# Performance work log

Hardware: AMD Instinct MI355X
Metric: run time of the kernel (lower is better)

Reference implementation:

```python
import jax, jax.numpy as jnp
import numpy as np

B, S, T, H, NH, G, E, I, R, L = 256, 256, 16, 1024, 8, 3, 8, 4096, 256, 3
GTEMP, RTEMP, TOPK_G, NEG = 1.0, 1.0, 2, -1e9

_W = {
    'ts_in_w': (3*H, H), 'ts_out_w': (H, H),
    'st_in_w': (3*H, H), 'st_out_w': (H, H),
    'ca_in_w': (3*H, H), 'ca_out_w': (H, H),
    'opq_w': (H, H), 'fuse_w': (H, 3*H), 'gate_w': (H, 3*H),
    'bs_w': (R, H), 'bt_w': (R, H), 'bo_w': (H, R),
    'cond_w': (H, 2*H), 'gr_w': (G, H), 'er_w': (G, E, H),
    'e_w1': (G, E, I, H), 'e_w2': (G, E, H, I), 'cls_w': (L, H),
}
_B = {
    'ts_in_b': (3*H,), 'ts_out_b': (H,), 'st_in_b': (3*H,), 'st_out_b': (H,),
    'ca_in_b': (3*H,), 'ca_out_b': (H,), 'fuse_b': (H,), 'gate_b': (H,),
    'bs_b': (R,), 'bt_b': (R,), 'bo_b': (H,), 'cond_b': (H,),
    'gr_b': (G,), 'er_b': (G, E), 'e_b1': (G, E, I), 'e_b2': (G, E, H),
    'cls_b': (L,), 'ln_b': (3*H,),
}


def setup_inputs() -> dict:
    key = jax.random.key(0)
    out = {}
    out['h_sent'] = jax.random.normal(jax.random.fold_in(key, 1), (B, S, H), dtype=jnp.float32)
    out['h_term'] = jax.random.normal(jax.random.fold_in(key, 2), (B, T, H), dtype=jnp.float32)
    for i, (name, shp) in enumerate(_W.items()):
        out[name] = 0.02 * jax.random.normal(jax.random.fold_in(key, 100 + i), shp, dtype=jnp.float32)
    for name, shp in _B.items():
        out[name] = jnp.zeros(shp, dtype=jnp.float32)
    out['ln_g'] = jnp.ones((3*H,), dtype=jnp.float32)
    return out


def _mha(q, k, v, w_in, b_in, w_out, b_out):
    # torch nn.MultiheadAttention (batch_first, eval mode / no dropout)
    wq, wk, wv = jnp.split(w_in, 3, axis=0)
    bq, bk, bv = jnp.split(b_in, 3, axis=0)
    Q, K, V = q @ wq.T + bq, k @ wk.T + bk, v @ wv.T + bv
    b, lq, _ = Q.shape
    lk = K.shape[1]
    d = H // NH
    Q = Q.reshape(b, lq, NH, d).transpose(0, 2, 1, 3)
    K = K.reshape(b, lk, NH, d).transpose(0, 2, 1, 3)
    V = V.reshape(b, lk, NH, d).transpose(0, 2, 1, 3)
    att = jax.nn.softmax(jnp.einsum('bhqd,bhkd->bhqk', Q, K) * (1.0 / d ** 0.5), axis=-1)
    o = jnp.einsum('bhqk,bhkd->bhqd', att, V).transpose(0, 2, 1, 3).reshape(b, lq, H)
    return o @ w_out.T + b_out


def _ln(x, g, b, eps=1e-5):
    mu = x.mean(-1, keepdims=True)
    var = ((x - mu) ** 2).mean(-1, keepdims=True)
    return (x - mu) * jax.lax.rsqrt(var + eps) * g + b


def reference(h_sent, h_term, ts_in_w, ts_in_b, ts_out_w, ts_out_b,
              st_in_w, st_in_b, st_out_w, st_out_b,
              ca_in_w, ca_in_b, ca_out_w, ca_out_b,
              opq_w, ln_g, ln_b, fuse_w, fuse_b, gate_w, gate_b,
              bs_w, bs_b, bt_w, bt_b, bo_w, bo_b, cond_w, cond_b,
              gr_w, gr_b, er_w, er_b, e_w1, e_b1, e_w2, e_b2, cls_w, cls_b):
    # --- co-attention fusion ---
    t2s = _mha(h_term, h_sent, h_sent, ts_in_w, ts_in_b, ts_out_w, ts_out_b)  # [B,T,H]
    s2t = _mha(h_sent, h_term, h_term, st_in_w, st_in_b, st_out_w, st_out_b)  # [B,S,H]
    v_term = t2s.mean(axis=1)   # [B,H]
    v_sent = s2t.mean(axis=1)   # [B,H]
    oq = h_term @ opq_w.T       # opinion query projection (no bias)
    v_op = _mha(oq, h_sent, h_sent, ca_in_w, ca_in_b, ca_out_w, ca_out_b).mean(axis=1)
    cat3 = jnp.concatenate([v_sent, v_term, v_op], axis=-1)        # [B,3H]
    fused_lin = _ln(cat3, ln_g, ln_b) @ fuse_w.T + fuse_b           # [B,H]
    g = jax.nn.sigmoid(cat3 @ gate_w.T + gate_b)                    # [B,H]
    bil = ((v_sent @ bs_w.T + bs_b) * (v_term @ bt_w.T + bt_b)) @ bo_w.T + bo_b
    fused = g * fused_lin + (1.0 - g) * bil                         # [B,H]
    cond = jnp.concatenate([fused, v_term], axis=-1) @ cond_w.T + cond_b  # [B,H]
    # --- hierarchical group -> expert soft routing ---
    glog = fused @ gr_w.T + gr_b                                    # [B,G]
    thr = jax.lax.top_k(glog, TOPK_G)[0][:, -1:]
    glog = jnp.where(glog >= thr, glog, NEG)
    gp = jax.nn.softmax(glog / GTEMP, axis=-1)                      # [B,G]
    elog = jnp.einsum('bh,geh->bge', cond, er_w) + er_b             # [B,G,E]
    ep = jax.nn.softmax(elog / RTEMP, axis=-1)
    # all experts applied densely (soft routing); FFN experts: GELU MLP
    h1 = jax.nn.gelu(jnp.einsum('bh,geih->bgei', fused, e_w1) + e_b1, approximate=False)
    y = jnp.einsum('bgei,gehi->bgeh', h1, e_w2) + e_b2              # [B,G,E,H]
    moe = jnp.einsum('bge,bgeh->bh', gp[:, :, None] * ep, y)
    out = fused + moe                                               # residual merge
    return out @ cls_w.T + cls_b                                    # [B,L]
```

## Files before the change

kernel.cpp:

```cpp
#include <hip/hip_runtime.h>
#include <math.h>


#define B_    256
#define S_    256
#define T_    16
#define H_    1024
#define NH_   8
#define DH_   128
#define M128_ 128
#define G_    3
#define E_    8
#define I_    4096
#define R_    256
#define L_    3
#define GE_   24

using bf16x8 = __attribute__((ext_vector_type(8))) __bf16;
using f32x4  = __attribute__((ext_vector_type(4))) float;

__device__ inline float wave_sum(float v) {
    for (int o = 32; o > 0; o >>= 1) v += __shfl_xor(v, o);
    return v;
}
__device__ inline float wave_max(float v) {
    for (int o = 32; o > 0; o >>= 1) v = fmaxf(v, __shfl_xor(v, o));
    return v;
}

template <int ACT, int NCH>
__global__ __launch_bounds__(256) void sgemm2_k(
    const float* __restrict__ Ap, const float* __restrict__ Bp,
    const float* __restrict__ biasp, const float* __restrict__ roffp,
    float* __restrict__ Cf,
    int K, int m2shift, int zshift, int z2max,
    long sA1, long sA2, long sAz1, long sAz2,
    long ldb, long sBz1, long sBz2, long sBia1, long sBia2,
    long sC1, long sC2, long sCz1, long sCz2, long sR1, long sR2,
    float scale)
{
    const int z  = blockIdx.z;
    const int z1 = z >> zshift;
    const int z2 = z & ((1 << zshift) - 1);
    if (z2 >= z2max) return;
    const int m2mask = (1 << m2shift) - 1;
    const int row0 = blockIdx.y * 128;
    const float* Ab = Ap + (long)z1 * sAz1 + (long)z2 * sAz2;
    const float* Bb = Bp + (long)z1 * sBz1 + (long)z2 * sBz2;
    const float* biasb = biasp ? biasp + (long)z1 * sBia1 + (long)z2 * sBia2 : nullptr;
    const float* roffb = roffp ? roffp + (long)z1 * sR1 + (long)z2 * sR2 : nullptr;

    __shared__ __bf16 Ahs[128 * 40];
    __shared__ __bf16 Als[128 * 40];
    __shared__ __bf16 Bhs[128 * 40];
    __shared__ __bf16 Bls[128 * 40];

    const int tid  = threadIdx.x;
    const int lane = tid & 63;
    const int wid  = tid >> 6;
    const int wm = (wid >> 1) * 64;
    const int wn = (wid & 1) * 64;
    const int fr  = lane & 15;
    const int fkb = (lane >> 4) * 16;
    const int qrow = tid >> 2;
    const int c4   = tid & 3;

    float4 pfa[2][2], pfb[2][2];

    auto loadAB = [&](int k0, int col0) {
#pragma unroll
        for (int rep = 0; rep < 2; ++rep) {
            const int row = qrow + rep * 64;
            const int r = row0 + row;
            const int r1 = r >> m2shift, r2 = r & m2mask;
            const float* srcA = Ab + (long)r1 * sA1 + (long)r2 * sA2 + k0 + c4 * 8;
            pfa[rep][0] = *(const float4*)srcA;
            pfa[rep][1] = *(const float4*)(srcA + 4);
            const float* srcB = Bb + (long)(col0 + row) * ldb + k0 + c4 * 8;
            pfb[rep][0] = *(const float4*)srcB;
            pfb[rep][1] = *(const float4*)(srcB + 4);
        }
    };

    for (int ch = 0; ch < NCH; ++ch) {
        const int col0 = (blockIdx.x * NCH + ch) * 128;
        f32x4 acc[4][4] = {};
        loadAB(0, col0);
        for (int k0 = 0; k0 < K; k0 += 32) {
            __syncthreads();
#pragma unroll
            for (int rep = 0; rep < 2; ++rep) {
                const int row = qrow + rep * 64;
                {
                    const float fv[8] = {pfa[rep][0].x, pfa[rep][0].y, pfa[rep][0].z, pfa[rep][0].w,
                                         pfa[rep][1].x, pfa[rep][1].y, pfa[rep][1].z, pfa[rep][1].w};
                    bf16x8 hi, lo;
#pragma unroll
                    for (int j = 0; j < 8; ++j) {
                        const __bf16 h = (__bf16)fv[j];
                        hi[j] = h; lo[j] = (__bf16)(fv[j] - (float)h);
                    }
                    *(bf16x8*)&Ahs[row * 40 + c4 * 8] = hi;
                    *(bf16x8*)&Als[row * 40 + c4 * 8] = lo;
                }
                {
                    const float fv[8] = {pfb[rep][0].x, pfb[rep][0].y, pfb[rep][0].z, pfb[rep][0].w,
                                         pfb[rep][1].x, pfb[rep][1].y, pfb[rep][1].z, pfb[rep][1].w};
                    bf16x8 hi, lo;
#pragma unroll
                    for (int j = 0; j < 8; ++j) {
                        const __bf16 h = (__bf16)fv[j];
                        hi[j] = h; lo[j] = (__bf16)(fv[j] - (float)h);
                    }
                    *(bf16x8*)&Bhs[row * 40 + c4 * 8] = hi;
                    *(bf16x8*)&Bls[row * 40 + c4 * 8] = lo;
                }
            }
            __syncthreads();
            if (k0 + 32 < K) loadAB(k0 + 32, col0);

            bf16x8 bh4[4], bl4[4];
#pragma unroll
            for (int n = 0; n < 4; ++n) {
                bh4[n] = *(const bf16x8*)((const char*)&Bhs[(wn + n * 16 + fr) * 40] + fkb);
                bl4[n] = *(const bf16x8*)((const char*)&Bls[(wn + n * 16 + fr) * 40] + fkb);
            }
#pragma unroll
            for (int m = 0; m < 4; ++m) {
                const bf16x8 ah = *(const bf16x8*)((const char*)&Ahs[(wm + m * 16 + fr) * 40] + fkb);
                const bf16x8 al = *(const bf16x8*)((const char*)&Als[(wm + m * 16 + fr) * 40] + fkb);
#pragma unroll
                for (int n = 0; n < 4; ++n) {
                    acc[m][n] = __builtin_amdgcn_mfma_f32_16x16x32_bf16(ah, bh4[n], acc[m][n], 0, 0, 0);
                    acc[m][n] = __builtin_amdgcn_mfma_f32_16x16x32_bf16(ah, bl4[n], acc[m][n], 0, 0, 0);
                    acc[m][n] = __builtin_amdgcn_mfma_f32_16x16x32_bf16(al, bh4[n], acc[m][n], 0, 0, 0);
                }
            }
        }

        float* Cfb = Cf + (long)z1 * sCz1 + (long)z2 * sCz2;
        const int lr4 = (lane >> 4) * 4;
#pragma unroll
        for (int m = 0; m < 4; ++m) {
#pragma unroll
            for (int r = 0; r < 4; ++r) {
                const int rr = row0 + wm + m * 16 + lr4 + r;
                const int r1 = rr >> m2shift, r2 = rr & m2mask;
                const float ro = roffb ? roffb[rr] : 0.f;
                const long cb = (long)r1 * sC1 + (long)r2 * sC2;
#pragma unroll
                for (int n = 0; n < 4; ++n) {
                    const int cc = col0 + wn + n * 16 + fr;
                    float v = (acc[m][n][r] + ro) * scale;
                    if (biasp) v += biasb[cc];
                    if (ACT == 2) v = 1.0f / (1.0f + expf(-v));
                    Cfb[cb + cc] = v;
                }
            }
        }
    }
}

static void sg2(hipStream_t s, int act, int nch, int z2max,
                const float* A, const float* B, const float* bias, const float* roff,
                float* C, int gx, int gy, int gz,
                int K, int m2shift, int zshift,
                long sA1, long sA2, long sAz1, long sAz2,
                long ldb, long sBz1, long sBz2, long sBia1, long sBia2,
                long sC1, long sC2, long sCz1, long sCz2, long sR1, long sR2,
                float scale)
{
    dim3 g(gx, gy, gz), b(256);
#define S2ARGS A, B, bias, roff, C, K, m2shift, zshift, z2max, sA1, sA2, sAz1, sAz2, \
               ldb, sBz1, sBz2, sBia1, sBia2, sC1, sC2, sCz1, sCz2, sR1, sR2, scale
    if (nch == 2)      sgemm2_k<0, 2><<<g, b, 0, s>>>(S2ARGS);
    else if (act == 2) sgemm2_k<2, 1><<<g, b, 0, s>>>(S2ARGS);
    else               sgemm2_k<0, 1><<<g, b, 0, s>>>(S2ARGS);
#undef S2ARGS
}

template <int ABF16, int BSING, int ACT, int WMUL, int OUTH>
__global__ __launch_bounds__(512) void sgemm256_k(
    const void* __restrict__ Ap, const float* __restrict__ Bp,
    const float* __restrict__ biasp, const float* __restrict__ wmulp,
    float* __restrict__ Cf, __bf16* __restrict__ Ch,
    int K, long sA1, long sAz, long ldb, long sBz, long sBz2, int bzshift,
    long sBias, long sC1, long sCz, long sWr, float scale)
{
    const int z    = blockIdx.z;
    const int col0 = blockIdx.x * 128;
    const int z1 = z >> bzshift;
    const int z2 = z - (z1 << bzshift);
    const float* Bb = Bp + (long)z1 * sBz + (long)z2 * sBz2;
    const float* biasb = biasp ? biasp + (long)z1 * sBias : nullptr;

    __shared__ __bf16 Ah[256 * 40];
    __shared__ __bf16 Al[ABF16 ? 64 : 256 * 40];
    __shared__ __bf16 Bh[128 * 40];
    __shared__ __bf16 Bl[BSING ? 64 : 128 * 40];

    const int tid  = threadIdx.x;
    const int lane = tid & 63;
    const int wid  = tid >> 6;
    const int wm = (wid >> 1) * 64;
    const int wn = (wid & 1) * 64;
    const int fr  = lane & 15;
    const int fkb = (lane >> 4) * 16;

    f32x4 acc[4][4] = {};
    bf16x8 pfah[2];
    float4 pfaf[2][2];
    float4 pfb[2];

    auto loadAB = [&](int k0) {
#pragma unroll
        for (int rep = 0; rep < 2; ++rep) {
            const int idx = tid + rep * 512;
            const int row = idx >> 2;
            const int cc4 = idx & 3;
            if (ABF16) {
                pfah[rep] = *(const bf16x8*)((const __bf16*)Ap + (long)z * sAz +
                                             (long)row * sA1 + k0 + cc4 * 8);
            } else {
                const float* src = (const float*)Ap + (long)z * sAz +
                                   (long)row * sA1 + k0 + cc4 * 8;
                pfaf[rep][0] = *(const float4*)src;
                pfaf[rep][1] = *(const float4*)(src + 4);
            }
        }
        {
            const int row = tid >> 2;
            const int cc4 = tid & 3;
            const float* src = Bb + (long)(col0 + row) * ldb + k0 + cc4 * 8;
            pfb[0] = *(const float4*)src;
            pfb[1] = *(const float4*)(src + 4);
        }
    };

    loadAB(0);
    for (int k0 = 0; k0 < K; k0 += 32) {
        __syncthreads();
#pragma unroll
        for (int rep = 0; rep < 2; ++rep) {
            const int idx = tid + rep * 512;
            const int row = idx >> 2;
            const int cc4 = idx & 3;
            if (ABF16) {
                *(bf16x8*)&Ah[row * 40 + cc4 * 8] = pfah[rep];
            } else {
                const float fv[8] = {pfaf[rep][0].x, pfaf[rep][0].y, pfaf[rep][0].z, pfaf[rep][0].w,
                                     pfaf[rep][1].x, pfaf[rep][1].y, pfaf[rep][1].z, pfaf[rep][1].w};
                bf16x8 hi, lo;
#pragma unroll
                for (int j = 0; j < 8; ++j) {
                    const __bf16 h = (__bf16)fv[j];
                    hi[j] = h; lo[j] = (__bf16)(fv[j] - (float)h);
                }
                *(bf16x8*)&Ah[row * 40 + cc4 * 8] = hi;
                *(bf16x8*)&Al[row * 40 + cc4 * 8] = lo;
            }
        }
        {
            const int row = tid >> 2;
            const int cc4 = tid & 3;
            const float fv[8] = {pfb[0].x, pfb[0].y, pfb[0].z, pfb[0].w,
                                 pfb[1].x, pfb[1].y, pfb[1].z, pfb[1].w};
            bf16x8 hi, lo;
#pragma unroll
            for (int j = 0; j < 8; ++j) {
                const __bf16 h = (__bf16)fv[j];
                hi[j] = h;
                if (!BSING) lo[j] = (__bf16)(fv[j] - (float)h);
            }
            *(bf16x8*)&Bh[row * 40 + cc4 * 8] = hi;
            if (!BSING) *(bf16x8*)&Bl[row * 40 + cc4 * 8] = lo;
        }
        __syncthreads();
        if (k0 + 32 < K) loadAB(k0 + 32);

        bf16x8 bh4[4], bl4[4];
#pragma unroll
        for (int n = 0; n < 4; ++n) {
            bh4[n] = *(const bf16x8*)((const char*)&Bh[(wn + n * 16 + fr) * 40] + fkb);
            if (!BSING) bl4[n] = *(const bf16x8*)((const char*)&Bl[(wn + n * 16 + fr) * 40] + fkb);
        }
#pragma unroll
        for (int m = 0; m < 4; ++m) {
            const bf16x8 ah = *(const bf16x8*)((const char*)&Ah[(wm + m * 16 + fr) * 40] + fkb);
            bf16x8 al;
            if (!ABF16) al = *(const bf16x8*)((const char*)&Al[(wm + m * 16 + fr) * 40] + fkb);
#pragma unroll
            for (int n = 0; n < 4; ++n) {
                acc[m][n] = __builtin_amdgcn_mfma_f32_16x16x32_bf16(ah, bh4[n], acc[m][n], 0, 0, 0);
                if (!BSING) acc[m][n] = __builtin_amdgcn_mfma_f32_16x16x32_bf16(ah, bl4[n], acc[m][n], 0, 0, 0);
                if (!ABF16) acc[m][n] = __builtin_amdgcn_mfma_f32_16x16x32_bf16(al, bh4[n], acc[m][n], 0, 0, 0);
            }
        }
    }

    const int lr4 = (lane >> 4) * 4;
#pragma unroll
    for (int m = 0; m < 4; ++m) {
#pragma unroll
        for (int r = 0; r < 4; ++r) {
            const int rr = wm + m * 16 + lr4 + r;
#pragma unroll
            for (int n = 0; n < 4; ++n) {
                const int cc = col0 + wn + n * 16 + fr;
                float v = acc[m][n][r] * scale;
                if (biasp) v += biasb[cc];
                if (ACT == 1) v = 0.5f * v * (1.0f + erff(v * 0.70710678118654752f));
                if (WMUL) v *= wmulp[(long)rr * sWr + z];
                if (OUTH) Ch[(long)z * sCz + (long)rr * sC1 + cc] = (__bf16)v;
                else      Cf[(long)z * sCz + (long)rr * sC1 + cc] = v;
            }
        }
    }
}

#define BM 64
#define BN 64
#define BK 16
__global__ __launch_bounds__(256) void gemm_k(
    const float* __restrict__ Ap, const float* __restrict__ Bp,
    const float* __restrict__ biasp, float* __restrict__ Cp,
    int M, int N, int K, long sA1, long ldb, long sC1)
{
    const int row0 = blockIdx.y * BM;
    const int col0 = blockIdx.x * BN;
    const int tid = threadIdx.x;
    __shared__ float As[BK][BM + 4];
    __shared__ float Bs[BK][BN + 4];
    float acc[4][4] = {};
    const int tm = (tid >> 4) << 2;
    const int tn = (tid & 15) << 2;
    for (int k0 = 0; k0 < K; k0 += BK) {
        {
            const int i = tid << 2;
            const int m = i >> 4, kk = i & 15;
            const int r = row0 + m;
            float4 v = make_float4(0.f, 0.f, 0.f, 0.f);
            if (r < M) v = *(const float4*)(Ap + (long)r * sA1 + k0 + kk);
            As[kk + 0][m] = v.x; As[kk + 1][m] = v.y;
            As[kk + 2][m] = v.z; As[kk + 3][m] = v.w;
        }
        {
            const int i = tid << 2;
            const int n = i >> 4, kk = i & 15;
            const int c = col0 + n;
            float4 v = make_float4(0.f, 0.f, 0.f, 0.f);
            if (c < N) v = *(const float4*)(Bp + (long)c * ldb + k0 + kk);
            Bs[kk + 0][n] = v.x; Bs[kk + 1][n] = v.y;
            Bs[kk + 2][n] = v.z; Bs[kk + 3][n] = v.w;
        }
        __syncthreads();
#pragma unroll
        for (int kk = 0; kk < BK; ++kk) {
            const float4 av = *(const float4*)&As[kk][tm];
            const float4 bv = *(const float4*)&Bs[kk][tn];
            acc[0][0] += av.x * bv.x; acc[0][1] += av.x * bv.y;
            acc[0][2] += av.x * bv.z; acc[0][3] += av.x * bv.w;
            acc[1][0] += av.y * bv.x; acc[1][1] += av.y * bv.y;
            acc[1][2] += av.y * bv.z; acc[1][3] += av.y * bv.w;
            acc[2][0] += av.z * bv.x; acc[2][1] += av.z * bv.y;
            acc[2][2] += av.z * bv.z; acc[2][3] += av.z * bv.w;
            acc[3][0] += av.w * bv.x; acc[3][1] += av.w * bv.y;
            acc[3][2] += av.w * bv.z; acc[3][3] += av.w * bv.w;
        }
        __syncthreads();
    }
#pragma unroll
    for (int i2 = 0; i2 < 4; ++i2) {
        const int r = row0 + tm + i2;
        if (r >= M) continue;
        float* crow = Cp + (long)r * sC1;
#pragma unroll
        for (int j = 0; j < 4; ++j) {
            const int c = col0 + tn + j;
            if (c >= N) continue;
            float v = acc[i2][j];
            if (biasp) v += biasp[c];
            crow[c] = v;
        }
    }
}

static void g_launch(hipStream_t s, const float* A, const float* Bw, const float* bias,
                     float* C, int M, int N, int K, long sA1, long ldb, long sC1)
{
    dim3 grid((N + BN - 1) / BN, (M + BM - 1) / BM, 1);
    gemm_k<<<grid, dim3(256), 0, s>>>(A, Bw, bias, C, M, N, K, sA1, ldb, sC1);
}

template <int ACT>
__global__ void kred_k(const float* __restrict__ part, const float* __restrict__ bias,
                       float* __restrict__ out, int n, long stride, int nz, int biasMask)
{
    const int i = blockIdx.x * blockDim.x + threadIdx.x;
    if (i >= n) return;
    float v = 0.f;
    for (int z = 0; z < nz; ++z) v += part[(long)z * stride + i];
    if (bias) v += bias[i & biasMask];
    if (ACT == 2) v = 1.0f / (1.0f + expf(-v));
    out[i] = v;
}

__global__ void cpy8_k(const float* s0, const float* s1, const float* s2, const float* s3,
                       const float* s4, const float* s5, const float* s6, const float* s7,
                       float* d0, float* d1, float* d2, float* d3,
                       float* d4, float* d5, float* d6, float* d7)
{
    const int seg = blockIdx.x >> 10;
    const int i = ((blockIdx.x & 1023) * 256 + threadIdx.x);
    const float* srcs[8] = {s0, s1, s2, s3, s4, s5, s6, s7};
    float* dsts[8] = {d0, d1, d2, d3, d4, d5, d6, d7};
    ((float4*)dsts[seg])[i] = ((const float4*)srcs[seg])[i];
}

__global__ void tT4_k(const float* s0, const float* s1, const float* s2, const float* s3,
                      float* d0, float* d1, float* d2, float* d3)
{
    __shared__ float t[32][33];
    const int seg = blockIdx.y >> 5;
    const float* src = seg == 0 ? s0 : seg == 1 ? s1 : seg == 2 ? s2 : s3;
    float* dst = seg == 0 ? d0 : seg == 1 ? d1 : seg == 2 ? d2 : d3;
    const int c0 = blockIdx.x * 32, r0 = (blockIdx.y & 31) * 32;
    const int tx = threadIdx.x & 31, ty = threadIdx.x >> 5;
#pragma unroll
    for (int i = 0; i < 4; ++i) {
        const int r = ty + i * 8;
        t[r][tx] = src[(long)(r0 + r) * 1024 + c0 + tx];
    }
    __syncthreads();
#pragma unroll
    for (int i = 0; i < 4; ++i) {
        const int r = ty + i * 8;
        dst[(long)(c0 + r) * 1024 + r0 + tx] = t[tx][r];
    }
}

__global__ void biascat_k(const float* __restrict__ ts_b, const float* __restrict__ ca_b,
                          const float* __restrict__ st_b,
                          const float* __restrict__ ts_ob, const float* __restrict__ ca_ob,
                          const float* __restrict__ st_ob,
                          float* __restrict__ BCAT, float* __restrict__ BKCAT,
                          float* __restrict__ WVB, float* __restrict__ WOB)
{
    const int i = blockIdx.x * blockDim.x + threadIdx.x;
    if (i >= 1024) return;
    BCAT[i] = ts_b[i]; BCAT[1024 + i] = ca_b[i];
    BCAT[2048 + i] = st_b[1024 + i]; BCAT[3072 + i] = st_b[2048 + i];
    BKCAT[i] = ts_b[1024 + i]; BKCAT[1024 + i] = ca_b[1024 + i]; BKCAT[2048 + i] = st_b[i];
    WVB[i] = ts_b[2048 + i]; WVB[1024 + i] = ca_b[2048 + i];
    WOB[i] = ts_ob[i]; WOB[1024 + i] = ca_ob[i]; WOB[2048 + i] = st_ob[i];
}

__global__ void headdot3_k(const float* __restrict__ QALL, const float* __restrict__ BKCAT,
                           float* __restrict__ out)
{
    const int idx = blockIdx.x * blockDim.x + threadIdx.x;
    if (idx >= 3 * B_ * T_ * NH_) return;
    const int mod = idx >> 15;
    const int b = (idx >> 7) & 255;
    const int t = (idx >> 3) & 15;
    const int h = idx & 7;
    const float* q = QALL + (long)(b * 16 + t) * 4096 + mod * 1024 + h * 128;
    const float* bb = BKCAT + mod * 1024 + h * 128;
    float sum = 0.f;
    for (int k = 0; k < DH_; ++k) sum += q[k] * bb[k];
    out[idx] = sum;
}

__global__ __launch_bounds__(64) void softpb_k(const float* __restrict__ sc3,
                                               float* __restrict__ pbar,
// ... 203 lines not shown
    for (int e = 0; e < E_; ++e) { v[e] = expf(p[e] - m); sum += v[e]; }
    const float w = gp[idx] / sum;
#pragma unroll
    for (int e = 0; e < E_; ++e) p[e] = v[e] * w;
}

__global__ void moefinal_k(const float* __restrict__ part, const float* __restrict__ fused,
                           const float* __restrict__ wsc, const float* __restrict__ e_b2,
                           float* __restrict__ res)
{
    const int idx = blockIdx.x * blockDim.x + threadIdx.x;
    if (idx >= B_ * H_) return;
    const int b = idx >> 10;
    const int h = idx & (H_ - 1);
    float acc = fused[idx];
#pragma unroll 8
    for (int z = 0; z < 48; ++z) acc += part[(long)z * (B_ * H_) + idx];
    float ba = 0.f;
#pragma unroll
    for (int ge = 0; ge < GE_; ++ge) ba += wsc[b * GE_ + ge] * e_b2[ge * H_ + h];
    res[idx] = acc + ba;
}

extern "C" void kernel_launch(void* const* d_in, const int* in_sizes, int n_in,
                              void* d_out, int out_size, void* d_ws, size_t ws_size,
                              hipStream_t stream)
{
    const float* h_sent  = (const float*)d_in[0];
    const float* h_term  = (const float*)d_in[1];
    const float* ts_in_w = (const float*)d_in[2];
    const float* ts_out_w= (const float*)d_in[3];
    const float* st_in_w = (const float*)d_in[4];
    const float* st_out_w= (const float*)d_in[5];
    const float* ca_in_w = (const float*)d_in[6];
    const float* ca_out_w= (const float*)d_in[7];
    const float* opq_w   = (const float*)d_in[8];
    const float* fuse_w  = (const float*)d_in[9];
    const float* gate_w  = (const float*)d_in[10];
    const float* bs_w    = (const float*)d_in[11];
    const float* bt_w    = (const float*)d_in[12];
    const float* bo_w    = (const float*)d_in[13];
    const float* cond_w  = (const float*)d_in[14];
    const float* gr_w    = (const float*)d_in[15];
    const float* er_w    = (const float*)d_in[16];
    const float* e_w1    = (const float*)d_in[17];
    const float* e_w2    = (const float*)d_in[18];
    const float* cls_w   = (const float*)d_in[19];
    const float* ts_in_b = (const float*)d_in[20];
    const float* ts_out_b= (const float*)d_in[21];
    const float* st_in_b = (const float*)d_in[22];
    const float* st_out_b= (const float*)d_in[23];
    const float* ca_in_b = (const float*)d_in[24];
    const float* ca_out_b= (const float*)d_in[25];
    const float* fuse_b  = (const float*)d_in[26];
    const float* gate_b  = (const float*)d_in[27];
    const float* bs_b    = (const float*)d_in[28];
    const float* bt_b    = (const float*)d_in[29];
    const float* bo_b    = (const float*)d_in[30];
    const float* cond_b  = (const float*)d_in[31];
    const float* gr_b    = (const float*)d_in[32];
    const float* er_b    = (const float*)d_in[33];
    const float* e_b1    = (const float*)d_in[34];
    const float* e_b2    = (const float*)d_in[35];
    const float* cls_b   = (const float*)d_in[36];
    const float* ln_b    = (const float*)d_in[37];
    const float* ln_g    = (const float*)d_in[38];
    (void)in_sizes; (void)n_in; (void)out_size; (void)ws_size;

    float* ws = (float*)d_ws;
    size_t off = 0;
    auto allocF = [&](size_t n) { float* p = ws + off; off += (n + 63) & ~(size_t)63; return p; };

    float* QALL  = allocF(16777216);
    float* WCAT  = allocF(4194304);
    float* BCAT  = allocF(4096);
    float* BKCAT = allocF(3072);
    float* wT3   = allocF(3145728);
    float* opqT  = allocF(1048576);
    float* WVCAT = allocF(2097152);
    float* WVB   = allocF(2048);
    float* WOCAT = allocF(3145728);
    float* WOB   = allocF(3072);
    float* OFFS3 = allocF(98304);
    float* BIG3  = allocF(100663296);
    float* SC3   = allocF(25165824);
    float* PBAR3 = allocF(1048576);
    float* CTXB3 = allocF(4194304);
    float* PARTC = allocF(16777216);
    float* OBAR3 = allocF(786432);
    float* VOUT3 = allocF(786432);
    float* ATTM  = allocF(32768);
    float* CAT3  = allocF(786432);
    float* LNC   = allocF(786432);
    float* FLIN  = allocF(262144);
    float* GATE  = allocF(262144);
    float* BSV   = allocF(65536);
    float* BTV   = allocF(65536);
    float* PROD  = allocF(65536);
    float* BIL   = allocF(262144);
    float* FUSED = allocF(262144);
    float* FUSEDH= allocF(131072);
    float* CATFV = allocF(524288);
    float* COND  = allocF(262144);
    float* GLOG  = allocF(1024);
    float* GP    = allocF(1024);
    float* ELOG  = allocF(8192);
    float* RES   = allocF(262144);
    float* PARTF = allocF(1048576);
    float* H1Wf  = allocF(12582912);
    float* PART  = allocF(12582912);
    __bf16* FUSEDbf = (__bf16*)FUSEDH;
    __bf16* H1W     = (__bf16*)H1Wf;
    float* VTERM = VOUT3;
    float* VOP   = VOUT3 + 262144;
    float* VSENT = VOUT3 + 524288;

    hipStream_t s = stream;
    const float rscale = 0.08838834764831845f;
    const int ZBIG = 1 << 30;

    cpy8_k<<<dim3(8 * 1024), dim3(256), 0, s>>>(
        ts_in_w, st_in_w + 1048576, st_in_w + 2097152, ts_in_w + 2097152,
        ca_in_w + 2097152, ts_out_w, ca_out_w, st_out_w,
        WCAT, WCAT + 2097152, WCAT + 3145728, WVCAT,
        WVCAT + 1048576, WOCAT, WOCAT + 1048576, WOCAT + 2097152);
    biascat_k<<<dim3(4), dim3(256), 0, s>>>(ts_in_b, ca_in_b, st_in_b,
                                            ts_out_b, ca_out_b, st_out_b,
                                            BCAT, BKCAT, WVB, WOB);
    tT4_k<<<dim3(32, 128), dim3(256), 0, s>>>(
        ts_in_w + 1048576, ca_in_w + 1048576, st_in_w, opq_w,
        wT3, wT3 + 1048576, wT3 + 2097152, opqT);

    sg2(s, 0, 1, ZBIG, ca_in_w, opqT, nullptr, nullptr, WCAT + 1048576,
        8, 8, 1, 1024, 12, 0, 0, 1024, 0, 0, 1024, 0, 0, 0, 0,
        0, 1024, 0, 0, 0, 0, 1.f);

    sg2(s, 0, 1, ZBIG, h_term, WCAT, BCAT, nullptr, QALL,
        32, 32, 1, 1024, 12, 0, 0, 1024, 0, 0, 1024, 0, 0, 0, 0,
        0, 4096, 0, 0, 0, 0, 1.f);

    headdot3_k<<<dim3(384), dim3(256), 0, s>>>(QALL, BKCAT, OFFS3);

    sg2(s, 0, 1, ZBIG, QALL, wT3, nullptr, nullptr, BIG3,
        8, 32, 24, 128, 4, 3,
        65536, 4096, 1024, 128,
        1024, 1048576, 128, 0, 0,
        131072, 8192, 33554432, 1024, 0, 0, 1.f);

    sg2(s, 0, 2, 3, BIG3, h_sent, nullptr, OFFS3, SC3,
        1, 1, 1024, 1024, 12, 2,
        0, 1024, 131072, 33554432,
        1024, 262144, 0, 0, 0,
        0, 256, 32768, 8388608, 128, 32768, rscale);

    softpb_k<<<dim3(3 * B_ * NH_), dim3(64), 0, s>>>(SC3, PBAR3, ATTM);

    ctxw2_k<<<dim3(B_, 4), dim3(256), 0, s>>>(PBAR3, h_sent, PARTC);
    kred_k<0><<<dim3(4194304 / 256), dim3(256), 0, s>>>(PARTC, nullptr, CTXB3,
                                                        4194304, 4194304, 4, 0);
    sg2(s, 0, 1, ZBIG, CTXB3, WVCAT, WVB, nullptr, OBAR3,
        1, 2, 16, 1024, 12, 3,
        0, 8192, 2097152, 1024,
        1024, 1048576, 131072, 1024, 128,
        0, 1024, 262144, 128, 0, 0, 1.f);

    ohead2_k<<<dim3((B_ * H_ + 255) / 256), dim3(256), 0, s>>>(ATTM, QALL, OBAR3 + 524288);

    sg2(s, 0, 1, ZBIG, OBAR3, WOCAT, WOB, nullptr, VOUT3,
        8, 2, 3, 1024, 12, 0,
        0, 1024, 262144, 0,
        1024, 1048576, 0, 1024, 0,
        0, 1024, 262144, 0, 0, 0, 1.f);

    cat3_k<<<dim3((B_ * 3 * H_ + 255) / 256), dim3(256), 0, s>>>(VSENT, VTERM, VOP, CAT3);
    ln_k<<<dim3(B_), dim3(256), 0, s>>>(CAT3, ln_g, ln_b, LNC);
    sg2(s, 0, 1, ZBIG, LNC, fuse_w, nullptr, nullptr, PARTF,
        8, 2, 4, 768, 12, 2, 0, 3072, 0, 768, 3072, 0, 768, 0, 0,
        0, 1024, 0, 262144, 0, 0, 1.f);
    kred_k<0><<<dim3(1024), dim3(256), 0, s>>>(PARTF, fuse_b, FLIN, 262144, 262144, 4, 1023);
    sg2(s, 0, 1, ZBIG, CAT3, gate_w, nullptr, nullptr, PARTF,
        8, 2, 4, 768, 12, 2, 0, 3072, 0, 768, 3072, 0, 768, 0, 0,
        0, 1024, 0, 262144, 0, 0, 1.f);
    kred_k<2><<<dim3(1024), dim3(256), 0, s>>>(PARTF, gate_b, GATE, 262144, 262144, 4, 1023);
    sg2(s, 0, 1, ZBIG, VSENT, bs_w, nullptr, nullptr, PARTF,
        2, 2, 4, 256, 12, 2, 0, 1024, 0, 256, 1024, 0, 256, 0, 0,
        0, 256, 0, 65536, 0, 0, 1.f);
    kred_k<0><<<dim3(256), dim3(256), 0, s>>>(PARTF, bs_b, BSV, 65536, 65536, 4, 255);
    sg2(s, 0, 1, ZBIG, VTERM, bt_w, nullptr, nullptr, PARTF,
        2, 2, 4, 256, 12, 2, 0, 1024, 0, 256, 1024, 0, 256, 0, 0,
        0, 256, 0, 65536, 0, 0, 1.f);
    kred_k<0><<<dim3(256), dim3(256), 0, s>>>(PARTF, bt_b, BTV, 65536, 65536, 4, 255);
    mulf_k<<<dim3((B_ * R_ + 255) / 256), dim3(256), 0, s>>>(BSV, BTV, PROD, B_ * R_);
    sg2(s, 0, 1, ZBIG, PROD, bo_w, nullptr, nullptr, PARTF,
        8, 2, 2, 128, 12, 1, 0, 256, 0, 128, 256, 0, 128, 0, 0,
        0, 1024, 0, 262144, 0, 0, 1.f);
    kred_k<0><<<dim3(1024), dim3(256), 0, s>>>(PARTF, bo_b, BIL, 262144, 262144, 2, 1023);
    fuse_k<<<dim3((B_ * H_ + 255) / 256), dim3(256), 0, s>>>(GATE, FLIN, BIL, FUSED, FUSEDbf);
    catfv_k<<<dim3((B_ * 2 * H_ + 255) / 256), dim3(256), 0, s>>>(FUSED, VTERM, CATFV);
    sg2(s, 0, 1, ZBIG, CATFV, cond_w, nullptr, nullptr, PARTF,
        8, 2, 4, 512, 12, 2, 0, 2048, 0, 512, 2048, 0, 512, 0, 0,
        0, 1024, 0, 262144, 0, 0, 1.f);
    kred_k<0><<<dim3(1024), dim3(256), 0, s>>>(PARTF, cond_b, COND, 262144, 262144, 4, 1023);

    g_launch(s, FUSED, gr_w, gr_b, GLOG, B_, G_, H_, H_, H_, G_);
    route_k<<<dim3(1), dim3(256), 0, s>>>(GLOG, GP);
    g_launch(s, COND, er_w, er_b, ELOG, B_, GE_, H_, H_, H_, GE_);
    epsm_k<<<dim3(3), dim3(256), 0, s>>>(ELOG, GP);

    sgemm256_k<1, 1, 1, 1, 1><<<dim3(I_ / 128, 1, GE_), dim3(512), 0, s>>>(
        FUSEDbf, e_w1, e_b1, ELOG, nullptr, H1W,
        1024, H_, 0, H_, (long)I_ * H_, 0, 0, I_,
        (long)GE_ * I_, I_, GE_, 1.f);
    sgemm256_k<1, 1, 0, 0, 0><<<dim3(H_ / 128, 1, 2 * GE_), dim3(512), 0, s>>>(
        H1W, e_w2, nullptr, nullptr, PART, nullptr,
        2048, (long)GE_ * I_, 2048, I_, (long)H_ * I_, 2048, 1, 0,
        H_, (long)B_ * H_, 0, 1.f);
    moefinal_k<<<dim3(B_ * H_ / 256), dim3(256), 0, s>>>(PART, FUSED, ELOG, e_b2, RES);

    g_launch(s, RES, cls_w, cls_b, (float*)d_out, B_, L_, H_, H_, H_, L_);
}
```

Before: 1.627 ms.

## Fuse projected-query and score GEMMs into one kernel, replace tiny GEMMs with dot kernels

Merges the two-stage score computation (QALL×wT3 into a large BIG3 buffer, then BIG3×h_sent) into a single fsc_k kernel. Each block computes its 128×64 projected tile in registers and keeps it in LDS as split bf16, so the roughly 400 MB intermediate is never written to or read back from global memory. The small routing and classifier GEMMs (N=3 or 24) move from a 64×64-tiled SIMT GEMM to one-wave-per-output dot-product kernels. Side changes: the NCH/z2max paths are removed from sgemm2_k and the bf16 hi/lo split is factored into a helper. The risk is that the fused kernel redoes the projection per block, uses a 512-thread launch with large LDS, and has a quarter of its blocks exit immediately.

```diff
diff --git a/kernel.cpp b/kernel.cpp
--- a/kernel.cpp
+++ b/kernel.cpp
@@ -28,12 +28,135 @@
     return v;
 }
 
-template <int ACT, int NCH>
+__device__ inline void split8(const float4& f0, const float4& f1, bf16x8& hi, bf16x8& lo)
+{
+    const float fv[8] = {f0.x, f0.y, f0.z, f0.w, f1.x, f1.y, f1.z, f1.w};
+#pragma unroll
+    for (int j = 0; j < 8; ++j) {
+        const __bf16 h = (__bf16)fv[j];
+        hi[j] = h; lo[j] = (__bf16)(fv[j] - (float)h);
+    }
+}
+
+__global__ __launch_bounds__(512) void fsc_k(
+    const float* __restrict__ QALL, const float* __restrict__ wT3,
+    const float* __restrict__ hs, const float* __restrict__ OFFS3,
+    float* __restrict__ SC3, float rscale)
+{
+    const int zz = ((blockIdx.z & 7) << 7) | (blockIdx.z >> 3);
+    const int b = zz >> 2, mod = zz & 3;
+    if (mod == 3) return;
+
+    __shared__ __bf16 A64h[128 * 72];
+    __shared__ __bf16 A64l[128 * 72];
+    __shared__ __bf16 Bh[128 * 40];
+    __shared__ __bf16 Bl[128 * 40];
+
+    const int tid  = threadIdx.x;
+    const int lane = tid & 63;
+    const int wid  = tid >> 6;
+    const int fr   = lane & 15;
+    const int fk   = lane >> 4;
+    const int wm2  = (wid >> 2) * 64;
+    const int wn2  = (wid & 3) * 32;
+
+    bf16x8 qh[4], ql[4];
+    {
+        const float* qb = QALL + ((long)(b * 16 + fr)) * 4096 + mod * 1024 + wid * 128;
+#pragma unroll
+        for (int jc = 0; jc < 4; ++jc) {
+            const float* p = qb + jc * 32 + fk * 8;
+            split8(*(const float4*)p, *(const float4*)(p + 4), qh[jc], ql[jc]);
+        }
+    }
+
+    f32x4 acc[2][4][2] = {};
+    const float* wbase = wT3 + (long)mod * 1048576 + wid * 128;
+    const float* hb = hs + (long)b * 262144;
+
+    for (int ks = 0; ks < 16; ++ks) {
+        __syncthreads();
+#pragma unroll
+        for (int nt = 0; nt < 4; ++nt) {
+            f32x4 pa = {};
+            const float* wr = wbase + (long)(ks * 64 + nt * 16 + fr) * 1024;
+#pragma unroll
+            for (int jc = 0; jc < 4; ++jc) {
+                const float* p = wr + jc * 32 + fk * 8;
+                bf16x8 wh, wl;
+                split8(*(const float4*)p, *(const float4*)(p + 4), wh, wl);
+                pa = __builtin_amdgcn_mfma_f32_16x16x32_bf16(qh[jc], wh, pa, 0, 0, 0);
+                pa = __builtin_amdgcn_mfma_f32_16x16x32_bf16(qh[jc], wl, pa, 0, 0, 0);
+                pa = __builtin_amdgcn_mfma_f32_16x16x32_bf16(ql[jc], wh, pa, 0, 0, 0);
+            }
+            const int kl = nt * 16 + fr;
+#pragma unroll
+            for (int r = 0; r < 4; ++r) {
+                const int m = (fk * 4 + r) * 8 + wid;
+                const float v = pa[r];
+                const __bf16 hv = (__bf16)v;
+                A64h[m * 72 + kl] = hv;
+                A64l[m * 72 + kl] = (__bf16)(v - (float)hv);
+            }
+        }
+#pragma unroll 1
+        for (int half = 0; half < 2; ++half) {
+#pragma unroll 1
+            for (int kc = 0; kc < 2; ++kc) {
+                __syncthreads();
+                {
+                    const int r2 = tid >> 2, q2 = tid & 3;
+                    const float* p = hb + (long)(half * 128 + r2) * 1024 +
+                                     ks * 64 + kc * 32 + q2 * 8;
+                    bf16x8 hh, hl;
+                    split8(*(const float4*)p, *(const float4*)(p + 4), hh, hl);
+                    *(bf16x8*)&Bh[r2 * 40 + q2 * 8] = hh;
+                    *(bf16x8*)&Bl[r2 * 40 + q2 * 8] = hl;
+                }
+                __syncthreads();
+                const int klo = kc * 32 + fk * 8;
+#pragma unroll
+                for (int mt = 0; mt < 4; ++mt) {
+                    const bf16x8 ah = *(const bf16x8*)&A64h[(wm2 + mt * 16 + fr) * 72 + klo];
+                    const bf16x8 al = *(const bf16x8*)&A64l[(wm2 + mt * 16 + fr) * 72 + klo];
+#pragma unroll
+                    for (int nt = 0; nt < 2; ++nt) {
+                        const bf16x8 bh = *(const bf16x8*)&Bh[(wn2 + nt * 16 + fr) * 40 + fk * 8];
+                        const bf16x8 bl = *(const bf16x8*)&Bl[(wn2 + nt * 16 + fr) * 40 + fk * 8];
+                        acc[half][mt][nt] = __builtin_amdgcn_mfma_f32_16x16x32_bf16(ah, bh, acc[half][mt][nt], 0, 0, 0);
+                        acc[half][mt][nt] = __builtin_amdgcn_mfma_f32_16x16x32_bf16(ah, bl, acc[half][mt][nt], 0, 0, 0);
+                        acc[half][mt][nt] = __builtin_amdgcn_mfma_f32_16x16x32_bf16(al, bh, acc[half][mt][nt], 0, 0, 0);
+                    }
+                }
+            }
+        }
+    }
+
+    float* out = SC3 + (long)mod * 8388608 + (long)b * 32768;
+    const float* ro = OFFS3 + mod * 32768 + b * 128;
+    const int lr4 = fk * 4;
+#pragma unroll
+    for (int half = 0; half < 2; ++half)
+#pragma unroll
+        for (int mt = 0; mt < 4; ++mt)
+#pragma unroll
+            for (int r = 0; r < 4; ++r) {
+                const int rr = wm2 + mt * 16 + lr4 + r;
+                const float rov = ro[rr];
+#pragma unroll
+                for (int nt = 0; nt < 2; ++nt) {
+                    const int cc = half * 128 + wn2 + nt * 16 + fr;
+                    out[(long)rr * 256 + cc] = (acc[half][mt][nt][r] + rov) * rscale;
+                }
+            }
+}
+
+template <int ACT>
 __global__ __launch_bounds__(256) void sgemm2_k(
     const float* __restrict__ Ap, const float* __restrict__ Bp,
     const float* __restrict__ biasp, const float* __restrict__ roffp,
     float* __restrict__ Cf,
-    int K, int m2shift, int zshift, int z2max,
+    int K, int m2shift, int zshift,
     long sA1, long sA2, long sAz1, long sAz2,
     long ldb, long sBz1, long sBz2, long sBia1, long sBia2,
     long sC1, long sC2, long sCz1, long sCz2, long sR1, long sR2,
@@ -42,9 +165,9 @@
     const int z  = blockIdx.z;
     const int z1 = z >> zshift;
     const int z2 = z & ((1 << zshift) - 1);
-    if (z2 >= z2max) return;
     const int m2mask = (1 << m2shift) - 1;
     const int row0 = blockIdx.y * 128;
+    const int col0 = blockIdx.x * 128;
     const float* Ab = Ap + (long)z1 * sAz1 + (long)z2 * sAz2;
     const float* Bb = Bp + (long)z1 * sBz1 + (long)z2 * sBz2;
     const float* biasb = biasp ? biasp + (long)z1 * sBia1 + (long)z2 * sBia2 : nullptr;
@@ -65,9 +188,10 @@
     const int qrow = tid >> 2;
     const int c4   = tid & 3;
 
+    f32x4 acc[4][4] = {};
     float4 pfa[2][2], pfb[2][2];
 
-    auto loadAB = [&](int k0, int col0) {
+    auto loadAB = [&](int k0) {
 #pragma unroll
         for (int rep = 0; rep < 2; ++rep) {
             const int row = qrow + rep * 64;
@@ -82,86 +206,65 @@
         }
     };
 
-    for (int ch = 0; ch < NCH; ++ch) {
-        const int col0 = (blockIdx.x * NCH + ch) * 128;
-        f32x4 acc[4][4] = {};
-        loadAB(0, col0);
-        for (int k0 = 0; k0 < K; k0 += 32) {
-            __syncthreads();
-#pragma unroll
-            for (int rep = 0; rep < 2; ++rep) {
-                const int row = qrow + rep * 64;
-                {
-                    const float fv[8] = {pfa[rep][0].x, pfa[rep][0].y, pfa[rep][0].z, pfa[rep][0].w,
-                                         pfa[rep][1].x, pfa[rep][1].y, pfa[rep][1].z, pfa[rep][1].w};
-                    bf16x8 hi, lo;
-#pragma unroll
-                    for (int j = 0; j < 8; ++j) {
-                        const __bf16 h = (__bf16)fv[j];
-                        hi[j] = h; lo[j] = (__bf16)(fv[j] - (float)h);
-                    }
-                    *(bf16x8*)&Ahs[row * 40 + c4 * 8] = hi;
-                    *(bf16x8*)&Als[row * 40 + c4 * 8] = lo;
-                }
-                {
-                    const float fv[8] = {pfb[rep][0].x, pfb[rep][0].y, pfb[rep][0].z, pfb[rep][0].w,
-                                         pfb[rep][1].x, pfb[rep][1].y, pfb[rep][1].z, pfb[rep][1].w};
-                    bf16x8 hi, lo;
-#pragma unroll
-                    for (int j = 0; j < 8; ++j) {
-                        const __bf16 h = (__bf16)fv[j];
-                        hi[j] = h; lo[j] = (__bf16)(fv[j] - (float)h);
-                    }
-                    *(bf16x8*)&Bhs[row * 40 + c4 * 8] = hi;
-                    *(bf16x8*)&Bls[row * 40 + c4 * 8] = lo;
-                }
+    loadAB(0);
+    for (int k0 = 0; k0 < K; k0 += 32) {
+        __syncthreads();
+#pragma unroll
+        for (int rep = 0; rep < 2; ++rep) {
+            const int row = qrow + rep * 64;
+            bf16x8 hi, lo;
+            split8(pfa[rep][0], pfa[rep][1], hi, lo);
+            *(bf16x8*)&Ahs[row * 40 + c4 * 8] = hi;
+            *(bf16x8*)&Als[row * 40 + c4 * 8] = lo;
+            split8(pfb[rep][0], pfb[rep][1], hi, lo);
+            *(bf16x8*)&Bhs[row * 40 + c4 * 8] = hi;
+            *(bf16x8*)&Bls[row * 40 + c4 * 8] = lo;
+        }
+        __syncthreads();
+        if (k0 + 32 < K) loadAB(k0 + 32);
+
+        bf16x8 bh4[4], bl4[4];
+#pragma unroll
+        for (int n = 0; n < 4; ++n) {
+            bh4[n] = *(const bf16x8*)((const char*)&Bhs[(wn + n * 16 + fr) * 40] + fkb);
+            bl4[n] = *(const bf16x8*)((const char*)&Bls[(wn + n * 16 + fr) * 40] + fkb);
+        }
+#pragma unroll
+        for (int m = 0; m < 4; ++m) {
+            const bf16x8 ah = *(const bf16x8*)((const char*)&Ahs[(wm + m * 16 + fr) * 40] + fkb);
+            const bf16x8 al = *(const bf16x8*)((const char*)&Als[(wm + m * 16 + fr) * 40] + fkb);
+#pragma unroll
+            for (int n = 0; n < 4; ++n) {
+                acc[m][n] = __builtin_amdgcn_mfma_f32_16x16x32_bf16(ah, bh4[n], acc[m][n], 0, 0, 0);
+                acc[m][n] = __builtin_amdgcn_mfma_f32_16x16x32_bf16(ah, bl4[n], acc[m][n], 0, 0, 0);
+                acc[m][n] = __builtin_amdgcn_mfma_f32_16x16x32_bf16(al, bh4[n], acc[m][n], 0, 0, 0);
             }
-            __syncthreads();
-            if (k0 + 32 < K) loadAB(k0 + 32, col0);
-
-            bf16x8 bh4[4], bl4[4];
+        }
+    }
+
+    float* Cfb = Cf + (long)z1 * sCz1 + (long)z2 * sCz2;
+    const int lr4 = (lane >> 4) * 4;
+#pragma unroll
+    for (int m = 0; m < 4; ++m) {
+#pragma unroll
+        for (int r = 0; r < 4; ++r) {
+            const int rr = row0 + wm + m * 16 + lr4 + r;
+            const int r1 = rr >> m2shift, r2 = rr & m2mask;
+            const float ro = roffb ? roffb[rr] : 0.f;
+            const long cb = (long)r1 * sC1 + (long)r2 * sC2;
 #pragma unroll
             for (int n = 0; n < 4; ++n) {
-                bh4[n] = *(const bf16x8*)((const char*)&Bhs[(wn + n * 16 + fr) * 40] + fkb);
-                bl4[n] = *(const bf16x8*)((const char*)&Bls[(wn + n * 16 + fr) * 40] + fkb);
+                const int cc = col0 + wn + n * 16 + fr;
+                float v = (acc[m][n][r] + ro) * scale;
+                if (biasp) v += biasb[cc];
+                if (ACT == 2) v = 1.0f / (1.0f + expf(-v));
+                Cfb[cb + cc] = v;
             }
-#pragma unroll
-            for (int m = 0; m < 4; ++m) {
-                const bf16x8 ah = *(const bf16x8*)((const char*)&Ahs[(wm + m * 16 + fr) * 40] + fkb);
-                const bf16x8 al = *(const bf16x8*)((const char*)&Als[(wm + m * 16 + fr) * 40] + fkb);
-#pragma unroll
-                for (int n = 0; n < 4; ++n) {
-                    acc[m][n] = __builtin_amdgcn_mfma_f32_16x16x32_bf16(ah, bh4[n], acc[m][n], 0, 0, 0);
-                    acc[m][n] = __builtin_amdgcn_mfma_f32_16x16x32_bf16(ah, bl4[n], acc[m][n], 0, 0, 0);
-                    acc[m][n] = __builtin_amdgcn_mfma_f32_16x16x32_bf16(al, bh4[n], acc[m][n], 0, 0, 0);
-                }
-            }
-        }
-
-        float* Cfb = Cf + (long)z1 * sCz1 + (long)z2 * sCz2;
-        const int lr4 = (lane >> 4) * 4;
-#pragma unroll
-        for (int m = 0; m < 4; ++m) {
-#pragma unroll
-            for (int r = 0; r < 4; ++r) {
-                const int rr = row0 + wm + m * 16 + lr4 + r;
-                const int r1 = rr >> m2shift, r2 = rr & m2mask;
-                const float ro = roffb ? roffb[rr] : 0.f;
-                const long cb = (long)r1 * sC1 + (long)r2 * sC2;
-#pragma unroll
-                for (int n = 0; n < 4; ++n) {
-                    const int cc = col0 + wn + n * 16 + fr;
-                    float v = (acc[m][n][r] + ro) * scale;
-                    if (biasp) v += biasb[cc];
-                    if (ACT == 2) v = 1.0f / (1.0f + expf(-v));
-                    Cfb[cb + cc] = v;
-                }
-            }
-        }
-    }
-}
-
-static void sg2(hipStream_t s, int act, int nch, int z2max,
+        }
+    }
+}
+
+static void sg2(hipStream_t s, int act,
                 const float* A, const float* B, const float* bias, const float* roff,
                 float* C, int gx, int gy, int gz,
                 int K, int m2shift, int zshift,
@@ -171,11 +274,10 @@
                 float scale)
 {
     dim3 g(gx, gy, gz), b(256);
-#define S2ARGS A, B, bias, roff, C, K, m2shift, zshift, z2max, sA1, sA2, sAz1, sAz2, \
+#define S2ARGS A, B, bias, roff, C, K, m2shift, zshift, sA1, sA2, sAz1, sAz2, \
                ldb, sBz1, sBz2, sBia1, sBia2, sC1, sC2, sCz1, sCz2, sR1, sR2, scale
-    if (nch == 2)      sgemm2_k<0, 2><<<g, b, 0, s>>>(S2ARGS);
-    else if (act == 2) sgemm2_k<2, 1><<<g, b, 0, s>>>(S2ARGS);
-    else               sgemm2_k<0, 1><<<g, b, 0, s>>>(S2ARGS);
+    if (act == 2) sgemm2_k<2><<<g, b, 0, s>>>(S2ARGS);
+    else          sgemm2_k<0><<<g, b, 0, s>>>(S2ARGS);
 #undef S2ARGS
 }
 
@@ -248,14 +350,8 @@
             if (ABF16) {
                 *(bf16x8*)&Ah[row * 40 + cc4 * 8] = pfah[rep];
             } else {
-                const float fv[8] = {pfaf[rep][0].x, pfaf[rep][0].y, pfaf[rep][0].z, pfaf[rep][0].w,
-                                     pfaf[rep][1].x, pfaf[rep][1].y, pfaf[rep][1].z, pfaf[rep][1].w};
                 bf16x8 hi, lo;
-#pragma unroll
-                for (int j = 0; j < 8; ++j) {
-                    const __bf16 h = (__bf16)fv[j];
-                    hi[j] = h; lo[j] = (__bf16)(fv[j] - (float)h);
-                }
+                split8(pfaf[rep][0], pfaf[rep][1], hi, lo);
                 *(bf16x8*)&Ah[row * 40 + cc4 * 8] = hi;
                 *(bf16x8*)&Al[row * 40 + cc4 * 8] = lo;
             }
@@ -263,15 +359,8 @@
         {
             const int row = tid >> 2;
             const int cc4 = tid & 3;
-            const float fv[8] = {pfb[0].x, pfb[0].y, pfb[0].z, pfb[0].w,
-                                 pfb[1].x, pfb[1].y, pfb[1].z, pfb[1].w};
             bf16x8 hi, lo;
-#pragma unroll
-            for (int j = 0; j < 8; ++j) {
-                const __bf16 h = (__bf16)fv[j];
-                hi[j] = h;
-                if (!BSING) lo[j] = (__bf16)(fv[j] - (float)h);
-            }
+            split8(pfb[0], pfb[1], hi, lo);
             *(bf16x8*)&Bh[row * 40 + cc4 * 8] = hi;
             if (!BSING) *(bf16x8*)&Bl[row * 40 + cc4 * 8] = lo;
         }
@@ -318,78 +407,24 @@
     }
 }
 
-#define BM 64
-#define BN 64
-#define BK 16
-__global__ __launch_bounds__(256) void gemm_k(
-    const float* __restrict__ Ap, const float* __restrict__ Bp,
-    const float* __restrict__ biasp, float* __restrict__ Cp,
-    int M, int N, int K, long sA1, long ldb, long sC1)
-{
-    const int row0 = blockIdx.y * BM;
-    const int col0 = blockIdx.x * BN;
-    const int tid = threadIdx.x;
-    __shared__ float As[BK][BM + 4];
-    __shared__ float Bs[BK][BN + 4];
-    float acc[4][4] = {};
-    const int tm = (tid >> 4) << 2;
-    const int tn = (tid & 15) << 2;
-    for (int k0 = 0; k0 < K; k0 += BK) {
-        {
-            const int i = tid << 2;
-            const int m = i >> 4, kk = i & 15;
-            const int r = row0 + m;
-            float4 v = make_float4(0.f, 0.f, 0.f, 0.f);
-            if (r < M) v = *(const float4*)(Ap + (long)r * sA1 + k0 + kk);
-            As[kk + 0][m] = v.x; As[kk + 1][m] = v.y;
-            As[kk + 2][m] = v.z; As[kk + 3][m] = v.w;
-        }
-        {
-            const int i = tid << 2;
-            const int n = i >> 4, kk = i & 15;
-            const int c = col0 + n;
-            float4 v = make_float4(0.f, 0.f, 0.f, 0.f);
-            if (c < N) v = *(const float4*)(Bp + (long)c * ldb + k0 + kk);
-            Bs[kk + 0][n] = v.x; Bs[kk + 1][n] = v.y;
-            Bs[kk + 2][n] = v.z; Bs[kk + 3][n] = v.w;
-        }
-        __syncthreads();
-#pragma unroll
-        for (int kk = 0; kk < BK; ++kk) {
-            const float4 av = *(const float4*)&As[kk][tm];
-            const float4 bv = *(const float4*)&Bs[kk][tn];
-            acc[0][0] += av.x * bv.x; acc[0][1] += av.x * bv.y;
-            acc[0][2] += av.x * bv.z; acc[0][3] += av.x * bv.w;
-            acc[1][0] += av.y * bv.x; acc[1][1] += av.y * bv.y;
-            acc[1][2] += av.y * bv.z; acc[1][3] += av.y * bv.w;
-            acc[2][0] += av.z * bv.x; acc[2][1] += av.z * bv.y;
-            acc[2][2] += av.z * bv.z; acc[2][3] += av.z * bv.w;
-            acc[3][0] += av.w * bv.x; acc[3][1] += av.w * bv.y;
-            acc[3][2] += av.w * bv.z; acc[3][3] += av.w * bv.w;
-        }
-        __syncthreads();
-    }
-#pragma unroll
-    for (int i2 = 0; i2 < 4; ++i2) {
-        const int r = row0 + tm + i2;
-        if (r >= M) continue;
-        float* crow = Cp + (long)r * sC1;
-#pragma unroll
-        for (int j = 0; j < 4; ++j) {
-            const int c = col0 + tn + j;
-            if (c >= N) continue;
-            float v = acc[i2][j];
-            if (biasp) v += biasp[c];
-            crow[c] = v;
-        }
-    }
-}
-
-static void g_launch(hipStream_t s, const float* A, const float* Bw, const float* bias,
-                     float* C, int M, int N, int K, long sA1, long ldb, long sC1)
-{
-    dim3 grid((N + BN - 1) / BN, (M + BM - 1) / BM, 1);
-    gemm_k<<<grid, dim3(256), 0, s>>>(A, Bw, bias, C, M, N, K, sA1, ldb, sC1);
+__global__ void dotk_k(const float* __restrict__ A, const float* __restrict__ Bw,
+                       const float* __restrict__ bias, float* __restrict__ out,
+                       int MN, int N, int K)
+{
+    const int idx = blockIdx.x * (blockDim.x >> 6) + (threadIdx.x >> 6);
+    if (idx >= MN) return;
+    const int m = idx / N, n = idx - m * N;
+    const int lane = threadIdx.x & 63;
+    const float* a = A + (long)m * K;
+    const float* bb = Bw + (long)n * K;
+    float s = 0.f;
+    for (int k = lane * 4; k < K; k += 256) {
+        const float4 av = *(const float4*)(a + k);
+        const float4 bv = *(const float4*)(bb + k);
+        s += av.x * bv.x + av.y * bv.y + av.z * bv.z + av.w * bv.w;
+    }
+    s = wave_sum(s);
+    if (lane == 0) out[idx] = s + (bias ? bias[n] : 0.f);
 }
 
 template <int ACT>
@@ -759,7 +794,6 @@
     float* WOCAT = allocF(3145728);
     float* WOB   = allocF(3072);
     float* OFFS3 = allocF(98304);
-    float* BIG3  = allocF(100663296);
     float* SC3   = allocF(25165824);
     float* PBAR3 = allocF(1048576);
     float* CTXB3 = allocF(4194304);
@@ -794,7 +828,6 @@
 
     hipStream_t s = stream;
     const float rscale = 0.08838834764831845f;
-    const int ZBIG = 1 << 30;
 
     cpy8_k<<<dim3(8 * 1024), dim3(256), 0, s>>>(
         ts_in_w, st_in_w + 1048576, st_in_w + 2097152, ts_in_w + 2097152,
@@ -808,34 +841,24 @@
         ts_in_w + 1048576, ca_in_w + 1048576, st_in_w, opq_w,
         wT3, wT3 + 1048576, wT3 + 2097152, opqT);
 
-    sg2(s, 0, 1, ZBIG, ca_in_w, opqT, nullptr, nullptr, WCAT + 1048576,
+    sg2(s, 0, ca_in_w, opqT, nullptr, nullptr, WCAT + 1048576,
         8, 8, 1, 1024, 12, 0, 0, 1024, 0, 0, 1024, 0, 0, 0, 0,
         0, 1024, 0, 0, 0, 0, 1.f);
 
-    sg2(s, 0, 1, ZBIG, h_term, WCAT, BCAT, nullptr, QALL,
+    sg2(s, 0, h_term, WCAT, BCAT, nullptr, QALL,
         32, 32, 1, 1024, 12, 0, 0, 1024, 0, 0, 1024, 0, 0, 0, 0,
         0, 4096, 0, 0, 0, 0, 1.f);
 
     headdot3_k<<<dim3(384), dim3(256), 0, s>>>(QALL, BKCAT, OFFS3);
 
-    sg2(s, 0, 1, ZBIG, QALL, wT3, nullptr, nullptr, BIG3,
-        8, 32, 24, 128, 4, 3,
-        65536, 4096, 1024, 128,
-        1024, 1048576, 128, 0, 0,
-        131072, 8192, 33554432, 1024, 0, 0, 1.f);
-
-    sg2(s, 0, 2, 3, BIG3, h_sent, nullptr, OFFS3, SC3,
-        1, 1, 1024, 1024, 12, 2,
-        0, 1024, 131072, 33554432,
-        1024, 262144, 0, 0, 0,
-        0, 256, 32768, 8388608, 128, 32768, rscale);
+    fsc_k<<<dim3(1, 1, 1024), dim3(512), 0, s>>>(QALL, wT3, h_sent, OFFS3, SC3, rscale);
 
     softpb_k<<<dim3(3 * B_ * NH_), dim3(64), 0, s>>>(SC3, PBAR3, ATTM);
 
     ctxw2_k<<<dim3(B_, 4), dim3(256), 0, s>>>(PBAR3, h_sent, PARTC);
     kred_k<0><<<dim3(4194304 / 256), dim3(256), 0, s>>>(PARTC, nullptr, CTXB3,
                                                         4194304, 4194304, 4, 0);
-    sg2(s, 0, 1, ZBIG, CTXB3, WVCAT, WVB, nullptr, OBAR3,
+    sg2(s, 0, CTXB3, WVCAT, WVB, nullptr, OBAR3,
         1, 2, 16, 1024, 12, 3,
         0, 8192, 2097152, 1024,
         1024, 1048576, 131072, 1024, 128,
@@ -843,7 +866,7 @@
 
     ohead2_k<<<dim3((B_ * H_ + 255) / 256), dim3(256), 0, s>>>(ATTM, QALL, OBAR3 + 524288);
 
-    sg2(s, 0, 1, ZBIG, OBAR3, WOCAT, WOB, nullptr, VOUT3,
+    sg2(s, 0, OBAR3, WOCAT, WOB, nullptr, VOUT3,
         8, 2, 3, 1024, 12, 0,
         0, 1024, 262144, 0,
         1024, 1048576, 0, 1024, 0,
@@ -851,37 +874,37 @@
 
     cat3_k<<<dim3((B_ * 3 * H_ + 255) / 256), dim3(256), 0, s>>>(VSENT, VTERM, VOP, CAT3);
     ln_k<<<dim3(B_), dim3(256), 0, s>>>(CAT3, ln_g, ln_b, LNC);
-    sg2(s, 0, 1, ZBIG, LNC, fuse_w, nullptr, nullptr, PARTF,
+    sg2(s, 0, LNC, fuse_w, nullptr, nullptr, PARTF,
         8, 2, 4, 768, 12, 2, 0, 3072, 0, 768, 3072, 0, 768, 0, 0,
         0, 1024, 0, 262144, 0, 0, 1.f);
     kred_k<0><<<dim3(1024), dim3(256), 0, s>>>(PARTF, fuse_b, FLIN, 262144, 262144, 4, 1023);
-    sg2(s, 0, 1, ZBIG, CAT3, gate_w, nullptr, nullptr, PARTF,
+    sg2(s, 0, CAT3, gate_w, nullptr, nullptr, PARTF,
         8, 2, 4, 768, 12, 2, 0, 3072, 0, 768, 3072, 0, 768, 0, 0,
         0, 1024, 0, 262144, 0, 0, 1.f);
     kred_k<2><<<dim3(1024), dim3(256), 0, s>>>(PARTF, gate_b, GATE, 262144, 262144, 4, 1023);
-    sg2(s, 0, 1, ZBIG, VSENT, bs_w, nullptr, nullptr, PARTF,
+    sg2(s, 0, VSENT, bs_w, nullptr, nullptr, PARTF,
         2, 2, 4, 256, 12, 2, 0, 1024, 0, 256, 1024, 0, 256, 0, 0,
         0, 256, 0, 65536, 0, 0, 1.f);
     kred_k<0><<<dim3(256), dim3(256), 0, s>>>(PARTF, bs_b, BSV, 65536, 65536, 4, 255);
-    sg2(s, 0, 1, ZBIG, VTERM, bt_w, nullptr, nullptr, PARTF,
+    sg2(s, 0, VTERM, bt_w, nullptr, nullptr, PARTF,
         2, 2, 4, 256, 12, 2, 0, 1024, 0, 256, 1024, 0, 256, 0, 0,
         0, 256, 0, 65536, 0, 0, 1.f);
     kred_k<0><<<dim3(256), dim3(256), 0, s>>>(PARTF, bt_b, BTV, 65536, 65536, 4, 255);
     mulf_k<<<dim3((B_ * R_ + 255) / 256), dim3(256), 0, s>>>(BSV, BTV, PROD, B_ * R_);
-    sg2(s, 0, 1, ZBIG, PROD, bo_w, nullptr, nullptr, PARTF,
+    sg2(s, 0, PROD, bo_w, nullptr, nullptr, PARTF,
         8, 2, 2, 128, 12, 1, 0, 256, 0, 128, 256, 0, 128, 0, 0,
         0, 1024, 0, 262144, 0, 0, 1.f);
     kred_k<0><<<dim3(1024), dim3(256), 0, s>>>(PARTF, bo_b, BIL, 262144, 262144, 2, 1023);
     fuse_k<<<dim3((B_ * H_ + 255) / 256), dim3(256), 0, s>>>(GATE, FLIN, BIL, FUSED, FUSEDbf);
     catfv_k<<<dim3((B_ * 2 * H_ + 255) / 256), dim3(256), 0, s>>>(FUSED, VTERM, CATFV);
-    sg2(s, 0, 1, ZBIG, CATFV, cond_w, nullptr, nullptr, PARTF,
+    sg2(s, 0, CATFV, cond_w, nullptr, nullptr, PARTF,
         8, 2, 4, 512, 12, 2, 0, 2048, 0, 512, 2048, 0, 512, 0, 0,
         0, 1024, 0, 262144, 0, 0, 1.f);
     kred_k<0><<<dim3(1024), dim3(256), 0, s>>>(PARTF, cond_b, COND, 262144, 262144, 4, 1023);
 
-    g_launch(s, FUSED, gr_w, gr_b, GLOG, B_, G_, H_, H_, H_, G_);
+    dotk_k<<<dim3(192), dim3(256), 0, s>>>(FUSED, gr_w, gr_b, GLOG, B_ * G_, G_, H_);
     route_k<<<dim3(1), dim3(256), 0, s>>>(GLOG, GP);
-    g_launch(s, COND, er_w, er_b, ELOG, B_, GE_, H_, H_, H_, GE_);
+    dotk_k<<<dim3(1536), dim3(256), 0, s>>>(COND, er_w, er_b, ELOG, B_ * GE_, GE_, H_);
     epsm_k<<<dim3(3), dim3(256), 0, s>>>(ELOG, GP);
 
     sgemm256_k<1, 1, 1, 1, 1><<<dim3(I_ / 128, 1, GE_), dim3(512), 0, s>>>(
@@ -894,5 +917,5 @@
         H_, (long)B_ * H_, 0, 1.f);
     moefinal_k<<<dim3(B_ * H_ / 256), dim3(256), 0, s>>>(PART, FUSED, ELOG, e_b2, RES);
 
-    g_launch(s, RES, cls_w, cls_b, (float*)d_out, B_, L_, H_, H_, H_, L_);
-}
+    dotk_k<<<dim3(192), dim3(256), 0, s>>>(RES, cls_w, cls_b, (float*)d_out, B_ * L_, L_, H_);
+}
```

New measurement: 2.518 ms. 1.55x slower.
